# Performance work log

Measured on AMD Instinct MI355X. Metric: run time of the kernel, lower is better.

## Reference

```python
import jax, jax.numpy as jnp
import numpy as np

ALPHA = 0.2  # LeakyReLU negative slope
N_NODES = 8192
IN_F = 512
OUT_F = 64


def setup_inputs() -> dict:
    key = jax.random.key(0)
    k1, k2, k3, k4, k5 = jax.random.split(key, 5)
    x = jax.random.normal(k1, (N_NODES, IN_F), dtype=jnp.float32)
    n = jax.random.normal(k2, (N_NODES, IN_F), dtype=jnp.float32)
    # nn.Linear default init scale ~ 1/sqrt(fan_in)
    W_tran = jax.random.normal(k3, (OUT_F, IN_F), dtype=jnp.float32) / np.sqrt(IN_F)
    w_att1 = jax.random.normal(k4, (OUT_F,), dtype=jnp.float32) / np.sqrt(OUT_F)
    w_att2 = jax.random.normal(k5, (OUT_F,), dtype=jnp.float32) / np.sqrt(OUT_F)
    return {"x": x, "n": n, "W_tran": W_tran, "w_att1": w_att1, "w_att2": w_att2}


def reference(x, n, W_tran, w_att1, w_att2):
    # h1: [N, out], h2: [N, out]
    h1 = x @ W_tran.T
    h2 = n @ W_tran.T
    # additive attention scores: a[i, j] = att1(h1)_i + att2(h2)_j  -> [N, N]
    s1 = h1 @ w_att1  # [N]
    s2 = h2 @ w_att2  # [N]
    a = s1[:, None] + s2[None, :]
    a = jnp.where(a >= 0, a, ALPHA * a)  # LeakyReLU
    attn = jax.nn.softmax(a, axis=1)     # Softmax(dim=1) over keys
    return attn @ h1  # [N, out]
```

## Files before the change

### kernel.cpp

```cpp
#include <hip/hip_runtime.h>
#include <math.h>

#define NN   8192
#define KF   512
#define DF   64
#define NCH  32
#define NCOL 130

__global__ __launch_bounds__(256) void k_main(const float* __restrict__ x,
        const float* __restrict__ nmat, const float* __restrict__ W,
        const float* __restrict__ w1, const float* __restrict__ w2,
        float* __restrict__ h1, float* __restrict__ s1, float* __restrict__ s2) {
    const int tid = threadIdx.x;
    if (blockIdx.x < 256) {
        __shared__ float xs[32][34];
        __shared__ float wt[32][64];
        const int row0 = blockIdx.x * 32;
        const int ty = tid >> 4, tx = tid & 15;
        const int sr = tid >> 3;
        const int sc = (tid & 7) * 4;
        const int wd = tid & 63;
        const int wg = tid >> 6;
        float4 xv  = *reinterpret_cast<const float4*>(x + (size_t)(row0 + sr) * KF + sc);
        float4 wv0 = *reinterpret_cast<const float4*>(W + (size_t)wd * KF + wg * 8);
        float4 wv1 = *reinterpret_cast<const float4*>(W + (size_t)wd * KF + wg * 8 + 4);
        float a00=0,a01=0,a02=0,a03=0,a10=0,a11=0,a12=0,a13=0;
        for (int kc = 0; kc < 16; ++kc) {
            __syncthreads();
            xs[sc+0][sr]=xv.x; xs[sc+1][sr]=xv.y; xs[sc+2][sr]=xv.z; xs[sc+3][sr]=xv.w;
            wt[wg*8+0][wd]=wv0.x; wt[wg*8+1][wd]=wv0.y; wt[wg*8+2][wd]=wv0.z; wt[wg*8+3][wd]=wv0.w;
            wt[wg*8+4][wd]=wv1.x; wt[wg*8+5][wd]=wv1.y; wt[wg*8+6][wd]=wv1.z; wt[wg*8+7][wd]=wv1.w;
            __syncthreads();
            if (kc < 15) {
                const int kk = (kc + 1) * 32;
                xv  = *reinterpret_cast<const float4*>(x + (size_t)(row0 + sr) * KF + kk + sc);
                wv0 = *reinterpret_cast<const float4*>(W + (size_t)wd * KF + kk + wg * 8);
                wv1 = *reinterpret_cast<const float4*>(W + (size_t)wd * KF + kk + wg * 8 + 4);
            }
            #pragma unroll
            for (int k = 0; k < 32; ++k) {
                const float2 a = *reinterpret_cast<const float2*>(&xs[k][ty * 2]);
                const float4 b = *reinterpret_cast<const float4*>(&wt[k][tx * 4]);
                a00 = fmaf(a.x, b.x, a00); a01 = fmaf(a.x, b.y, a01);
                a02 = fmaf(a.x, b.z, a02); a03 = fmaf(a.x, b.w, a03);
                a10 = fmaf(a.y, b.x, a10); a11 = fmaf(a.y, b.y, a11);
                a12 = fmaf(a.y, b.z, a12); a13 = fmaf(a.y, b.w, a13);
            }
        }
        const int r0 = row0 + ty * 2;
        *reinterpret_cast<float4*>(h1 + (size_t)r0 * DF + tx * 4)       = make_float4(a00, a01, a02, a03);
        *reinterpret_cast<float4*>(h1 + (size_t)(r0 + 1) * DF + tx * 4) = make_float4(a10, a11, a12, a13);
        const float4 wv = *reinterpret_cast<const float4*>(w1 + tx * 4);
        float p0 = a00 * wv.x + a01 * wv.y + a02 * wv.z + a03 * wv.w;
        float p1 = a10 * wv.x + a11 * wv.y + a12 * wv.z + a13 * wv.w;
        #pragma unroll
        for (int off = 1; off < 16; off <<= 1) { p0 += __shfl_xor(p0, off); p1 += __shfl_xor(p1, off); }
        if (tx == 0) { s1[r0] = p0; s1[r0 + 1] = p1; }
    } else {
        __shared__ float v2s[KF];
        const int row0 = (blockIdx.x - 256) * 32;
        float a0 = 0.f, a1 = 0.f;
        for (int d = 0; d < DF; ++d) {
            const float wd2 = w2[d];
            a0 = fmaf(W[(size_t)d * KF + tid],       wd2, a0);
            a1 = fmaf(W[(size_t)d * KF + 256 + tid], wd2, a1);
        }
        v2s[tid] = a0; v2s[tid + 256] = a1;
        __syncthreads();
        const int lane = tid & 63, w = tid >> 6;
        const float4 b0 = *reinterpret_cast<const float4*>(&v2s[lane * 4]);
        const float4 b1 = *reinterpret_cast<const float4*>(&v2s[256 + lane * 4]);
        for (int rr = 0; rr < 8; ++rr) {
            const int row = row0 + w * 8 + rr;
            const float4 n0 = *reinterpret_cast<const float4*>(nmat + (size_t)row * KF + lane * 4);
            const float4 n1 = *reinterpret_cast<const float4*>(nmat + (size_t)row * KF + 256 + lane * 4);
            float acc = n0.x * b0.x;
            acc = fmaf(n0.y, b0.y, acc); acc = fmaf(n0.z, b0.z, acc); acc = fmaf(n0.w, b0.w, acc);
            acc = fmaf(n1.x, b1.x, acc); acc = fmaf(n1.y, b1.y, acc);
            acc = fmaf(n1.z, b1.z, acc); acc = fmaf(n1.w, b1.w, acc);
            #pragma unroll
            for (int off = 32; off; off >>= 1) acc += __shfl_xor(acc, off);
            if (lane == 0) s2[row] = acc;
        }
    }
}

__global__ __launch_bounds__(256) void k_rank(const float* __restrict__ s2,
        int* __restrict__ order, float* __restrict__ s2s,
        double* __restrict__ wpos, double* __restrict__ wneg) {
    __shared__ float sk[NN];
    __shared__ int part[256];
    const int tid = threadIdx.x;
    {
        const float4* src = reinterpret_cast<const float4*>(s2);
        float4* dst = reinterpret_cast<float4*>(sk);
        #pragma unroll
        for (int t = 0; t < 8; ++t) dst[tid + t * 256] = src[tid + t * 256];
    }
    __syncthreads();
    const int jl = tid & 15, seg = tid >> 4;
    const int j = blockIdx.x * 16 + jl;
    const float mine = sk[j];
    const int base = seg * 512;
    int cnt = 0;
    for (int q = 0; q < 128; ++q) {
        const int e = (q * 4 + seg * 4) & 511;
        const int idx = base + e;
        const float4 v = *reinterpret_cast<const float4*>(&sk[idx]);
        cnt += (v.x < mine) | ((v.x == mine) & (idx     < j));
        cnt += (v.y < mine) | ((v.y == mine) & (idx + 1 < j));
        cnt += (v.z < mine) | ((v.z == mine) & (idx + 2 < j));
        cnt += (v.w < mine) | ((v.w == mine) & (idx + 3 < j));
    }
    part[tid] = cnt;
    __syncthreads();
    if (tid < 16) {
        int r = 0;
        #pragma unroll
        for (int s = 0; s < 16; ++s) r += part[s * 16 + tid];
        const float v = mine;
        order[r] = blockIdx.x * 16 + tid;
        s2s[r] = v;
        wpos[r] = exp((double)v);
        wneg[r] = exp(0.2 * (double)v);
    }
}

__global__ __launch_bounds__(256) void k_gather(const float* __restrict__ h1,
        const int* __restrict__ order, float* __restrict__ h1sT) {
    __shared__ float t[64][65];
    const int lane = threadIdx.x & 63, w = threadIdx.x >> 6;
    const int r0 = blockIdx.x * 64;
    for (int i = 0; i < 16; ++i) {
        const int lr = w * 16 + i;
        const int row = order[r0 + lr];
        t[lr][lane] = h1[(size_t)row * DF + lane];
    }
    __syncthreads();
    for (int i = 0; i < 16; ++i) {
        const int dd = w * 16 + i;
        h1sT[(size_t)dd * NN + r0 + lane] = t[lane][dd];
    }
}

__global__ __launch_bounds__(256) void k_chunksum(const float* __restrict__ h1sT,
        const double* __restrict__ wpos, const double* __restrict__ wneg,
        double* __restrict__ cT) {
    const int col = blockIdx.x >> 5, c = blockIdx.x & 31;
    const int p = c * 256 + threadIdx.x;
    const int d = (col < 65) ? col : col - 65;
    const double wgt = (col < 65) ? wpos[p] : wneg[p];
    double val = (d < DF) ? wgt * (double)h1sT[(size_t)d * NN + p] : wgt;
    #pragma unroll
    for (int off = 32; off; off >>= 1) val += __shfl_xor(val, off);
    __shared__ double red[4];
    const int lane = threadIdx.x & 63, w = threadIdx.x >> 6;
    if (lane == 0) red[w] = val;
    __syncthreads();
    if (threadIdx.x == 0) cT[blockIdx.x] = red[0] + red[1] + red[2] + red[3];
}

__global__ __launch_bounds__(256) void k_scan(const float* __restrict__ h1sT,
        const double* __restrict__ wpos, const double* __restrict__ wneg,
        const double* __restrict__ cT, double* __restrict__ E) {
    const int col = blockIdx.x >> 5, c = blockIdx.x & 31;
    const int tid = threadIdx.x, lane = tid & 63, w = tid >> 6;
    const int p = c * 256 + tid;
    const int d = (col < 65) ? col : col - 65;
    const double wgt = (col < 65) ? wpos[p] : wneg[p];
    const double val = (d < DF) ? wgt * (double)h1sT[(size_t)d * NN + p] : wgt;
    double cOv = 0.0;
    for (int cc = 0; cc < c; ++cc) cOv += cT[(size_t)col * NCH + cc];
    double incl = val;
    #pragma unroll
    for (int off = 1; off < 64; off <<= 1) {
        double tv = __shfl_up(incl, off);
        if (lane >= off) incl += tv;
    }
    __shared__ double wtot[4];
    if (lane == 63) wtot[w] = incl;
    __syncthreads();
    double woff = cOv;
    for (int ww = 0; ww < w; ++ww) woff += wtot[ww];
    E[(size_t)p * NCOL + col] = woff + incl - val;
    if (c == NCH - 1 && tid == 255) E[(size_t)NN * NCOL + col] = woff + incl;
}

__global__ __launch_bounds__(256) void k_out(const float* __restrict__ s1,
        const float* __restrict__ s2s, const double* __restrict__ E,
        float* __restrict__ out) {
    const int lane = threadIdx.x & 63, wave = threadIdx.x >> 6;
    const int i = blockIdx.x * 4 + wave;
    const float s1v = s1[i];
    const float t = -s1v;
    int lo = 0, hi = NN;
    while (lo < hi) {
        int mid = (lo + hi) >> 1;
        if (s2s[mid] < t) lo = mid + 1; else hi = mid;
    }
    const double* Ek = E + (size_t)lo * NCOL;
    const double* Et = E + (size_t)NN * NCOL;
    const double e1 = exp((double)s1v);
    const double e2 = exp(0.2 * (double)s1v);
    const double num = e1 * (Et[lane] - Ek[lane]) + e2 * Ek[65 + lane];
    const double den = e1 * (Et[DF] - Ek[DF]) + e2 * Ek[65 + DF];
    out[(size_t)i * DF + lane] = (float)(num / den);
}

extern "C" void kernel_launch(void* const* d_in, const int* in_sizes, int n_in,
                              void* d_out, int out_size, void* d_ws, size_t ws_size,
                              hipStream_t stream) {
    const float* x    = (const float*)d_in[0];
    const float* nmat = (const float*)d_in[1];
    const float* W    = (const float*)d_in[2];
    const float* w1   = (const float*)d_in[3];
    const float* w2   = (const float*)d_in[4];
    float* out = (float*)d_out;

    char* ws = (char*)d_ws;
    size_t off = 0;
    auto alloc = [&](size_t bytes) -> void* {
        void* p = ws + off;
        off += (bytes + 255) & ~(size_t)255;
        return p;
    };
    float*  h1    = (float*)alloc((size_t)NN * DF * 4);
    float*  h1sT  = (float*)alloc((size_t)DF * NN * 4);
    float*  s1    = (float*)alloc((size_t)NN * 4);
    float*  s2    = (float*)alloc((size_t)NN * 4);
    int*    order = (int*)alloc((size_t)NN * 4);
    float*  s2s   = (float*)alloc((size_t)NN * 4);
    double* wpos  = (double*)alloc((size_t)NN * 8);
    double* wneg  = (double*)alloc((size_t)NN * 8);
    double* cT    = (double*)alloc((size_t)NCOL * NCH * 8);
    double* E     = (double*)alloc((size_t)(NN + 1) * NCOL * 8);

    k_main<<<512, 256, 0, stream>>>(x, nmat, W, w1, w2, h1, s1, s2);
    k_rank<<<512, 256, 0, stream>>>(s2, order, s2s, wpos, wneg);
    k_gather<<<128, 256, 0, stream>>>(h1, order, h1sT);
    k_chunksum<<<NCOL * NCH, 256, 0, stream>>>(h1sT, wpos, wneg, cT);
    k_scan<<<NCOL * NCH, 256, 0, stream>>>(h1sT, wpos, wneg, cT, E);
    k_out<<<NN / 4, 256, 0, stream>>>(s1, s2s, E, out);
}
```

Measured before the change: 79.98 us.

## Fuse gather into scan kernels, widen GEMM tile, use integer sort keys

Several changes land together. The k_gather transpose kernel is removed, and the chunk-sum and scan kernels now read h1 rows through order directly, handling 8 columns per block over a 17x32 grid instead of one column per block over 4160 blocks. The h1 GEMM goes from a 2x4 to a 4x4 register tile with 64-row blocks, and the E row stride is padded to 136. Ranking compares float values mapped to monotone unsigned keys instead of float compares. The changes cut launches, the h1sT round trip and redundant per-column loads, but they raise register pressure and make the E stores strided.

Result: slower. 87.05 us (+8.8%).

```diff
diff --git a/kernel.cpp b/kernel.cpp
--- a/kernel.cpp
+++ b/kernel.cpp
@@ -1,64 +1,72 @@
 #include <hip/hip_runtime.h>
 #include <math.h>
 
-#define NN   8192
-#define KF   512
-#define DF   64
-#define NCH  32
-#define NCOL 130
+#define NN    8192
+#define KF    512
+#define DF    64
+#define NCH   32
+#define EC    136
 
 __global__ __launch_bounds__(256) void k_main(const float* __restrict__ x,
         const float* __restrict__ nmat, const float* __restrict__ W,
         const float* __restrict__ w1, const float* __restrict__ w2,
         float* __restrict__ h1, float* __restrict__ s1, float* __restrict__ s2) {
     const int tid = threadIdx.x;
-    if (blockIdx.x < 256) {
-        __shared__ float xs[32][34];
+    if (blockIdx.x < 128) {
+        __shared__ float xs[32][68];
         __shared__ float wt[32][64];
-        const int row0 = blockIdx.x * 32;
+        const int row0 = blockIdx.x * 64;
         const int ty = tid >> 4, tx = tid & 15;
         const int sr = tid >> 3;
         const int sc = (tid & 7) * 4;
         const int wd = tid & 63;
         const int wg = tid >> 6;
-        float4 xv  = *reinterpret_cast<const float4*>(x + (size_t)(row0 + sr) * KF + sc);
+        float4 xv0 = *reinterpret_cast<const float4*>(x + (size_t)(row0 + sr) * KF + sc);
+        float4 xv1 = *reinterpret_cast<const float4*>(x + (size_t)(row0 + 32 + sr) * KF + sc);
         float4 wv0 = *reinterpret_cast<const float4*>(W + (size_t)wd * KF + wg * 8);
         float4 wv1 = *reinterpret_cast<const float4*>(W + (size_t)wd * KF + wg * 8 + 4);
-        float a00=0,a01=0,a02=0,a03=0,a10=0,a11=0,a12=0,a13=0;
+        float acc[4][4] = {};
         for (int kc = 0; kc < 16; ++kc) {
             __syncthreads();
-            xs[sc+0][sr]=xv.x; xs[sc+1][sr]=xv.y; xs[sc+2][sr]=xv.z; xs[sc+3][sr]=xv.w;
+            xs[sc+0][sr]=xv0.x; xs[sc+1][sr]=xv0.y; xs[sc+2][sr]=xv0.z; xs[sc+3][sr]=xv0.w;
+            xs[sc+0][32+sr]=xv1.x; xs[sc+1][32+sr]=xv1.y; xs[sc+2][32+sr]=xv1.z; xs[sc+3][32+sr]=xv1.w;
             wt[wg*8+0][wd]=wv0.x; wt[wg*8+1][wd]=wv0.y; wt[wg*8+2][wd]=wv0.z; wt[wg*8+3][wd]=wv0.w;
             wt[wg*8+4][wd]=wv1.x; wt[wg*8+5][wd]=wv1.y; wt[wg*8+6][wd]=wv1.z; wt[wg*8+7][wd]=wv1.w;
             __syncthreads();
             if (kc < 15) {
                 const int kk = (kc + 1) * 32;
-                xv  = *reinterpret_cast<const float4*>(x + (size_t)(row0 + sr) * KF + kk + sc);
+                xv0 = *reinterpret_cast<const float4*>(x + (size_t)(row0 + sr) * KF + kk + sc);
+                xv1 = *reinterpret_cast<const float4*>(x + (size_t)(row0 + 32 + sr) * KF + kk + sc);
                 wv0 = *reinterpret_cast<const float4*>(W + (size_t)wd * KF + kk + wg * 8);
                 wv1 = *reinterpret_cast<const float4*>(W + (size_t)wd * KF + kk + wg * 8 + 4);
             }
             #pragma unroll
             for (int k = 0; k < 32; ++k) {
-                const float2 a = *reinterpret_cast<const float2*>(&xs[k][ty * 2]);
-                const float4 b = *reinterpret_cast<const float4*>(&wt[k][tx * 4]);
-                a00 = fmaf(a.x, b.x, a00); a01 = fmaf(a.x, b.y, a01);
-                a02 = fmaf(a.x, b.z, a02); a03 = fmaf(a.x, b.w, a03);
-                a10 = fmaf(a.y, b.x, a10); a11 = fmaf(a.y, b.y, a11);
-                a12 = fmaf(a.y, b.z, a12); a13 = fmaf(a.y, b.w, a13);
+                const float4 a4 = *reinterpret_cast<const float4*>(&xs[k][ty * 4]);
+                const float4 b4 = *reinterpret_cast<const float4*>(&wt[k][tx * 4]);
+                const float av[4] = {a4.x, a4.y, a4.z, a4.w};
+                const float bv[4] = {b4.x, b4.y, b4.z, b4.w};
+                #pragma unroll
+                for (int i = 0; i < 4; ++i)
+                    #pragma unroll
+                    for (int j = 0; j < 4; ++j)
+                        acc[i][j] = fmaf(av[i], bv[j], acc[i][j]);
             }
         }
-        const int r0 = row0 + ty * 2;
-        *reinterpret_cast<float4*>(h1 + (size_t)r0 * DF + tx * 4)       = make_float4(a00, a01, a02, a03);
-        *reinterpret_cast<float4*>(h1 + (size_t)(r0 + 1) * DF + tx * 4) = make_float4(a10, a11, a12, a13);
         const float4 wv = *reinterpret_cast<const float4*>(w1 + tx * 4);
-        float p0 = a00 * wv.x + a01 * wv.y + a02 * wv.z + a03 * wv.w;
-        float p1 = a10 * wv.x + a11 * wv.y + a12 * wv.z + a13 * wv.w;
-        #pragma unroll
-        for (int off = 1; off < 16; off <<= 1) { p0 += __shfl_xor(p0, off); p1 += __shfl_xor(p1, off); }
-        if (tx == 0) { s1[r0] = p0; s1[r0 + 1] = p1; }
+        #pragma unroll
+        for (int i = 0; i < 4; ++i) {
+            const int r = row0 + ty * 4 + i;
+            *reinterpret_cast<float4*>(h1 + (size_t)r * DF + tx * 4) =
+                make_float4(acc[i][0], acc[i][1], acc[i][2], acc[i][3]);
+            float p = acc[i][0] * wv.x + acc[i][1] * wv.y + acc[i][2] * wv.z + acc[i][3] * wv.w;
+            #pragma unroll
+            for (int off = 1; off < 16; off <<= 1) p += __shfl_xor(p, off);
+            if (tx == 0) s1[r] = p;
+        }
     } else {
         __shared__ float v2s[KF];
-        const int row0 = (blockIdx.x - 256) * 32;
+        const int row0 = (blockIdx.x - 128) * 32;
         float a0 = 0.f, a1 = 0.f;
         for (int d = 0; d < DF; ++d) {
             const float wd2 = w2[d];
@@ -85,32 +93,40 @@
     }
 }
 
+__device__ __forceinline__ unsigned int f2key(float f) {
+    unsigned int u = __float_as_uint(f);
+    return u ^ ((u >> 31) ? 0xFFFFFFFFu : 0x80000000u);
+}
+
 __global__ __launch_bounds__(256) void k_rank(const float* __restrict__ s2,
         int* __restrict__ order, float* __restrict__ s2s,
         double* __restrict__ wpos, double* __restrict__ wneg) {
-    __shared__ float sk[NN];
+    __shared__ unsigned int sk[NN];
     __shared__ int part[256];
     const int tid = threadIdx.x;
     {
         const float4* src = reinterpret_cast<const float4*>(s2);
-        float4* dst = reinterpret_cast<float4*>(sk);
-        #pragma unroll
-        for (int t = 0; t < 8; ++t) dst[tid + t * 256] = src[tid + t * 256];
+        #pragma unroll
+        for (int t = 0; t < 8; ++t) {
+            const float4 v = src[tid + t * 256];
+            const int b = (tid + t * 256) * 4;
+            sk[b] = f2key(v.x); sk[b+1] = f2key(v.y); sk[b+2] = f2key(v.z); sk[b+3] = f2key(v.w);
+        }
     }
     __syncthreads();
     const int jl = tid & 15, seg = tid >> 4;
     const int j = blockIdx.x * 16 + jl;
-    const float mine = sk[j];
+    const unsigned int mk = sk[j];
     const int base = seg * 512;
     int cnt = 0;
     for (int q = 0; q < 128; ++q) {
         const int e = (q * 4 + seg * 4) & 511;
         const int idx = base + e;
-        const float4 v = *reinterpret_cast<const float4*>(&sk[idx]);
-        cnt += (v.x < mine) | ((v.x == mine) & (idx     < j));
-        cnt += (v.y < mine) | ((v.y == mine) & (idx + 1 < j));
-        cnt += (v.z < mine) | ((v.z == mine) & (idx + 2 < j));
-        cnt += (v.w < mine) | ((v.w == mine) & (idx + 3 < j));
+        const uint4 v = *reinterpret_cast<const uint4*>(&sk[idx]);
+        cnt += (v.x < mk) | ((v.x == mk) & (idx     < j));
+        cnt += (v.y < mk) | ((v.y == mk) & (idx + 1 < j));
+        cnt += (v.z < mk) | ((v.z == mk) & (idx + 2 < j));
+        cnt += (v.w < mk) | ((v.w == mk) & (idx + 3 < j));
     }
     part[tid] = cnt;
     __syncthreads();
@@ -118,72 +134,91 @@
         int r = 0;
         #pragma unroll
         for (int s = 0; s < 16; ++s) r += part[s * 16 + tid];
-        const float v = mine;
-        order[r] = blockIdx.x * 16 + tid;
+        const int jj = blockIdx.x * 16 + tid;
+        const float v = s2[jj];
+        order[r] = jj;
         s2s[r] = v;
         wpos[r] = exp((double)v);
         wneg[r] = exp(0.2 * (double)v);
     }
 }
 
-__global__ __launch_bounds__(256) void k_gather(const float* __restrict__ h1,
-        const int* __restrict__ order, float* __restrict__ h1sT) {
-    __shared__ float t[64][65];
-    const int lane = threadIdx.x & 63, w = threadIdx.x >> 6;
-    const int r0 = blockIdx.x * 64;
-    for (int i = 0; i < 16; ++i) {
-        const int lr = w * 16 + i;
-        const int row = order[r0 + lr];
-        t[lr][lane] = h1[(size_t)row * DF + lane];
-    }
-    __syncthreads();
-    for (int i = 0; i < 16; ++i) {
-        const int dd = w * 16 + i;
-        h1sT[(size_t)dd * NN + r0 + lane] = t[lane][dd];
-    }
-}
-
-__global__ __launch_bounds__(256) void k_chunksum(const float* __restrict__ h1sT,
-        const double* __restrict__ wpos, const double* __restrict__ wneg,
-        double* __restrict__ cT) {
-    const int col = blockIdx.x >> 5, c = blockIdx.x & 31;
-    const int p = c * 256 + threadIdx.x;
-    const int d = (col < 65) ? col : col - 65;
-    const double wgt = (col < 65) ? wpos[p] : wneg[p];
-    double val = (d < DF) ? wgt * (double)h1sT[(size_t)d * NN + p] : wgt;
-    #pragma unroll
-    for (int off = 32; off; off >>= 1) val += __shfl_xor(val, off);
-    __shared__ double red[4];
-    const int lane = threadIdx.x & 63, w = threadIdx.x >> 6;
-    if (lane == 0) red[w] = val;
-    __syncthreads();
-    if (threadIdx.x == 0) cT[blockIdx.x] = red[0] + red[1] + red[2] + red[3];
-}
-
-__global__ __launch_bounds__(256) void k_scan(const float* __restrict__ h1sT,
-        const double* __restrict__ wpos, const double* __restrict__ wneg,
-        const double* __restrict__ cT, double* __restrict__ E) {
-    const int col = blockIdx.x >> 5, c = blockIdx.x & 31;
+__device__ __forceinline__ void load_vals(int g, int p, const float* __restrict__ h1,
+        const int* __restrict__ order, const double* __restrict__ wpos,
+        const double* __restrict__ wneg, double* vals, int& ncols, int& colbase) {
+    if (g < 16) {
+        ncols = 8;
+        const int d0 = (g < 8) ? 8 * g : 8 * (g - 8);
+        colbase = (g < 8) ? d0 : 64 + d0;
+        const double wgt = (g < 8) ? wpos[p] : wneg[p];
+        const float* hp = h1 + (size_t)order[p] * DF + d0;
+        const float4 h0 = *reinterpret_cast<const float4*>(hp);
+        const float4 h4 = *reinterpret_cast<const float4*>(hp + 4);
+        vals[0]=wgt*h0.x; vals[1]=wgt*h0.y; vals[2]=wgt*h0.z; vals[3]=wgt*h0.w;
+        vals[4]=wgt*h4.x; vals[5]=wgt*h4.y; vals[6]=wgt*h4.z; vals[7]=wgt*h4.w;
+    } else {
+        ncols = 2; colbase = 128;
+        vals[0] = wpos[p]; vals[1] = wneg[p];
+    }
+}
+
+__global__ __launch_bounds__(256) void k_csum(const float* __restrict__ h1,
+        const int* __restrict__ order, const double* __restrict__ wpos,
+        const double* __restrict__ wneg, double* __restrict__ cT) {
+    const int g = blockIdx.x, c = blockIdx.y;
     const int tid = threadIdx.x, lane = tid & 63, w = tid >> 6;
     const int p = c * 256 + tid;
-    const int d = (col < 65) ? col : col - 65;
-    const double wgt = (col < 65) ? wpos[p] : wneg[p];
-    const double val = (d < DF) ? wgt * (double)h1sT[(size_t)d * NN + p] : wgt;
-    double cOv = 0.0;
-    for (int cc = 0; cc < c; ++cc) cOv += cT[(size_t)col * NCH + cc];
-    double incl = val;
-    #pragma unroll
-    for (int off = 1; off < 64; off <<= 1) {
-        double tv = __shfl_up(incl, off);
-        if (lane >= off) incl += tv;
-    }
-    __shared__ double wtot[4];
-    if (lane == 63) wtot[w] = incl;
-    __syncthreads();
-    double woff = cOv;
-    for (int ww = 0; ww < w; ++ww) woff += wtot[ww];
-    E[(size_t)p * NCOL + col] = woff + incl - val;
-    if (c == NCH - 1 && tid == 255) E[(size_t)NN * NCOL + col] = woff + incl;
+    double vals[8]; int ncols, colbase;
+    load_vals(g, p, h1, order, wpos, wneg, vals, ncols, colbase);
+    __shared__ double red[4][8];
+    for (int jj = 0; jj < ncols; ++jj) {
+        double r = vals[jj];
+        #pragma unroll
+        for (int off = 32; off; off >>= 1) r += __shfl_xor(r, off);
+        if (lane == 0) red[w][jj] = r;
+    }
+    __syncthreads();
+    if (tid < ncols)
+        cT[(size_t)(colbase + tid) * NCH + c] = red[0][tid] + red[1][tid] + red[2][tid] + red[3][tid];
+}
+
+__global__ __launch_bounds__(256) void k_scan(const float* __restrict__ h1,
+        const int* __restrict__ order, const double* __restrict__ wpos,
+        const double* __restrict__ wneg, const double* __restrict__ cT,
+        double* __restrict__ E) {
+    const int g = blockIdx.x, c = blockIdx.y;
+    const int tid = threadIdx.x, lane = tid & 63, w = tid >> 6;
+    const int p = c * 256 + tid;
+    double vals[8], inc8[8]; int ncols, colbase;
+    load_vals(g, p, h1, order, wpos, wneg, vals, ncols, colbase);
+    __shared__ double cOs[8];
+    __shared__ double wtot[4][8];
+    if (tid < ncols) {
+        double s = 0.0;
+        const double* ct = cT + (size_t)(colbase + tid) * NCH;
+        for (int cc = 0; cc < c; ++cc) s += ct[cc];
+        cOs[tid] = s;
+    }
+    for (int jj = 0; jj < ncols; ++jj) {
+        double incl = vals[jj];
+        #pragma unroll
+        for (int off = 1; off < 64; off <<= 1) {
+            double t = __shfl_up(incl, off);
+            if (lane >= off) incl += t;
+        }
+        inc8[jj] = incl;
+        if (lane == 63) wtot[w][jj] = incl;
+    }
+    __syncthreads();
+    double* Ep = E + (size_t)p * EC + colbase;
+    for (int jj = 0; jj < ncols; ++jj) {
+        double woff = cOs[jj];
+        for (int ww = 0; ww < w; ++ww) woff += wtot[ww][jj];
+        Ep[jj] = woff + inc8[jj] - vals[jj];
+    }
+    if (c == NCH - 1 && tid < ncols)
+        E[(size_t)NN * EC + colbase + tid] =
+            cOs[tid] + wtot[0][tid] + wtot[1][tid] + wtot[2][tid] + wtot[3][tid];
 }
 
 __global__ __launch_bounds__(256) void k_out(const float* __restrict__ s1,
@@ -198,12 +233,12 @@
         int mid = (lo + hi) >> 1;
         if (s2s[mid] < t) lo = mid + 1; else hi = mid;
     }
-    const double* Ek = E + (size_t)lo * NCOL;
-    const double* Et = E + (size_t)NN * NCOL;
+    const double* Ek = E + (size_t)lo * EC;
+    const double* Et = E + (size_t)NN * EC;
     const double e1 = exp((double)s1v);
     const double e2 = exp(0.2 * (double)s1v);
-    const double num = e1 * (Et[lane] - Ek[lane]) + e2 * Ek[65 + lane];
-    const double den = e1 * (Et[DF] - Ek[DF]) + e2 * Ek[65 + DF];
+    const double num = e1 * (Et[lane] - Ek[lane]) + e2 * Ek[64 + lane];
+    const double den = e1 * (Et[128] - Ek[128]) + e2 * Ek[129];
     out[(size_t)i * DF + lane] = (float)(num / den);
 }
 
@@ -225,20 +260,18 @@
         return p;
     };
     float*  h1    = (float*)alloc((size_t)NN * DF * 4);
-    float*  h1sT  = (float*)alloc((size_t)DF * NN * 4);
     float*  s1    = (float*)alloc((size_t)NN * 4);
     float*  s2    = (float*)alloc((size_t)NN * 4);
     int*    order = (int*)alloc((size_t)NN * 4);
     float*  s2s   = (float*)alloc((size_t)NN * 4);
     double* wpos  = (double*)alloc((size_t)NN * 8);
     double* wneg  = (double*)alloc((size_t)NN * 8);
-    double* cT    = (double*)alloc((size_t)NCOL * NCH * 8);
-    double* E     = (double*)alloc((size_t)(NN + 1) * NCOL * 8);
-
-    k_main<<<512, 256, 0, stream>>>(x, nmat, W, w1, w2, h1, s1, s2);
+    double* cT    = (double*)alloc((size_t)130 * NCH * 8);
+    double* E     = (double*)alloc((size_t)(NN + 1) * EC * 8);
+
+    k_main<<<384, 256, 0, stream>>>(x, nmat, W, w1, w2, h1, s1, s2);
     k_rank<<<512, 256, 0, stream>>>(s2, order, s2s, wpos, wneg);
-    k_gather<<<128, 256, 0, stream>>>(h1, order, h1sT);
-    k_chunksum<<<NCOL * NCH, 256, 0, stream>>>(h1sT, wpos, wneg, cT);
-    k_scan<<<NCOL * NCH, 256, 0, stream>>>(h1sT, wpos, wneg, cT, E);
+    k_csum<<<dim3(17, NCH), 256, 0, stream>>>(h1, order, wpos, wneg, cT);
+    k_scan<<<dim3(17, NCH), 256, 0, stream>>>(h1, order, wpos, wneg, cT, E);
     k_out<<<NN / 4, 256, 0, stream>>>(s1, s2s, E, out);
 }
```
